# Performance work log

Measured on AMD Instinct MI355X. Metric: run time of the kernel, lower is better.

The kernel has to match this reference:

```python
import jax, jax.numpy as jnp
import numpy as np

BN_EPS = 1e-5
NUM_GRAPHS = 256


def _bn(h, g, b):
    # training-mode batch norm over the node dimension
    m = jnp.mean(h, axis=0)
    v = jnp.var(h, axis=0)
    return g * (h - m) * jax.lax.rsqrt(v + BN_EPS) + b


def setup_inputs() -> dict:
    key = jax.random.key(0)
    ks = jax.random.split(key, 24)
    N, E, F, H, H3 = 50000, 800000, 64, 128, 512
    C, R, L1 = 256, H + H + H3, 1024  # num_classes, readout dim 768, lin1 width

    def w(k, shape):
        return (jax.random.normal(k, shape, jnp.float32) / np.float32(np.sqrt(shape[0])))

    return {
        "x": jax.random.normal(ks[0], (N, F), jnp.float32),
        "edge_index": jax.random.randint(ks[1], (2, E), 0, N, jnp.int32),
        "batch": jnp.sort(jax.random.randint(ks[2], (N,), 0, NUM_GRAPHS, jnp.int32)),
        # conv1 MLP: Linear(F,H) ReLU Linear(H,H); BN1
        "w1a": w(ks[3], (F, H)), "b1a": jnp.zeros((H,), jnp.float32),
        "w1b": w(ks[4], (H, H)), "b1b": jnp.zeros((H,), jnp.float32),
        "g1": jnp.ones((H,), jnp.float32), "bt1": jnp.zeros((H,), jnp.float32),
        # conv2 MLP: Linear(H,H) ReLU Linear(H,H); BN2
        "w2a": w(ks[5], (H, H)), "b2a": jnp.zeros((H,), jnp.float32),
        "w2b": w(ks[6], (H, H)), "b2b": jnp.zeros((H,), jnp.float32),
        "g2": jnp.ones((H,), jnp.float32), "bt2": jnp.zeros((H,), jnp.float32),
        # conv3 MLP: Linear(H,512) ReLU; BN3
        "w3": w(ks[7], (H, H3)), "b3": jnp.zeros((H3,), jnp.float32),
        "g3": jnp.ones((H3,), jnp.float32), "bt3": jnp.zeros((H3,), jnp.float32),
        # readout MLP
        "wl1": w(ks[8], (R, L1)), "bl1": jnp.zeros((L1,), jnp.float32),
        "wl2": w(ks[9], (L1, C)), "bl2": jnp.zeros((C,), jnp.float32),
    }


def reference(x, edge_index, batch,
              w1a, b1a, w1b, b1b, g1, bt1,
              w2a, b2a, w2b, b2b, g2, bt2,
              w3, b3, g3, bt3,
              wl1, bl1, wl2, bl2):
    src, dst = edge_index[0], edge_index[1]
    N = x.shape[0]

    def agg(h):  # GIN aggregation, eps=0: x_i + sum_{j->i} x_j
        return h + jax.ops.segment_sum(h[src], dst, num_segments=N)

    h1 = jax.nn.relu(_bn(jax.nn.relu(agg(x) @ w1a + b1a) @ w1b + b1b, g1, bt1))
    h2 = jax.nn.relu(_bn(jax.nn.relu(agg(h1) @ w2a + b2a) @ w2b + b2b, g2, bt2))
    h3 = jax.nn.relu(_bn(jax.nn.relu(agg(h2) @ w3 + b3), g3, bt3))

    def pool(h):  # global_add_pool
        return jax.ops.segment_sum(h, batch, num_segments=NUM_GRAPHS)

    h = jnp.concatenate([pool(h1), pool(h2), pool(h3)], axis=1)  # [G, 768]
    return jax.nn.relu(h @ wl1 + bl1) @ wl2 + bl2  # [G, num_classes]
```

## Files before the change

### kernel.cpp

```cpp
#include <hip/hip_runtime.h>

#define DEV_INLINE __device__ __forceinline__

DEV_INLINE void fma4(float4& a, float s, const float4& w) {
  a.x = fmaf(s, w.x, a.x);
  a.y = fmaf(s, w.y, a.y);
  a.z = fmaf(s, w.z, a.z);
  a.w = fmaf(s, w.w, a.w);
}

DEV_INLINE float4 xform4(const float4& v, const float4& sc, const float4& sh) {
  float4 r;
  r.x = fmaxf(fmaf(v.x, sc.x, sh.x), 0.f);
  r.y = fmaxf(fmaf(v.y, sc.y, sh.y), 0.f);
  r.z = fmaxf(fmaf(v.z, sc.z, sh.z), 0.f);
  r.w = fmaxf(fmaf(v.w, sc.w, sh.w), 0.f);
  return r;
}

DEV_INLINE void atomAddF(float* p, float v) { unsafeAtomicAdd(p, v); }

__global__ void hist_kernel(const int* __restrict__ dst, int* __restrict__ deg, int E) {
  int i = blockIdx.x * blockDim.x + threadIdx.x;
  int st = gridDim.x * blockDim.x;
  for (; i < E; i += st) atomicAdd(&deg[dst[i]], 1);
}

__global__ __launch_bounds__(1024) void scan_kernel(const int* __restrict__ deg,
                                                    int* __restrict__ rowStart,
                                                    int* __restrict__ cursor, int N) {
  __shared__ int part[1024];
  const int t = threadIdx.x;
  const int chunk = (N + 1023) / 1024;
  const int base = t * chunk;
  int s = 0;
  for (int i = 0; i < chunk; ++i) {
    int idx = base + i;
    if (idx < N) s += deg[idx];
  }
  part[t] = s;
  __syncthreads();
  for (int off = 1; off < 1024; off <<= 1) {
    int u = (t >= off) ? part[t - off] : 0;
    __syncthreads();
    part[t] += u;
    __syncthreads();
  }
  int running = part[t] - s;
  for (int i = 0; i < chunk; ++i) {
    int idx = base + i;
    if (idx < N) {
      rowStart[idx] = running;
      cursor[idx] = running;
      running += deg[idx];
    }
  }
  if (t == 1023) rowStart[N] = part[1023];
}

__global__ void fill_kernel(const int* __restrict__ src, const int* __restrict__ dst,
                            int* __restrict__ cursor, int* __restrict__ adj, int E) {
  int i = blockIdx.x * blockDim.x + threadIdx.x;
  int st = gridDim.x * blockDim.x;
  for (; i < E; i += st) {
    int slot = atomicAdd(&cursor[dst[i]], 1);
    adj[slot] = src[i];
  }
}

template <int CH4, bool XF>
__global__ __launch_bounds__(256) void gather_kernel(const float* __restrict__ h,
                                                     const int* __restrict__ rowStart,
                                                     const int* __restrict__ adj,
                                                     const float* __restrict__ ss,
                                                     float* __restrict__ agg, int N) {
  constexpr int H = CH4 * 4;
  constexpr int NPB = 256 / CH4;
  const int t = threadIdx.x;
  const int c4 = t % CH4;
  const int nl = t / CH4;
  const int node = blockIdx.x * NPB + nl;
  if (node >= N) return;
  const int c = c4 * 4;
  float4 sc, sh;
  if (XF) {
    sc = *reinterpret_cast<const float4*>(ss + c);
    sh = *reinterpret_cast<const float4*>(ss + H + c);
  }
  float4 acc = *reinterpret_cast<const float4*>(h + (long long)node * H + c);
  if (XF) acc = xform4(acc, sc, sh);
  const int e1 = rowStart[node + 1];
  for (int i = rowStart[node]; i < e1; ++i) {
    int s = adj[i];
    float4 u = *reinterpret_cast<const float4*>(h + (long long)s * H + c);
    if (XF) u = xform4(u, sc, sh);
    acc.x += u.x; acc.y += u.y; acc.z += u.z; acc.w += u.w;
  }
  *reinterpret_cast<float4*>(agg + (long long)node * H + c) = acc;
}

template <int K, int NC, bool RELU, bool STATS>
__global__ __launch_bounds__(256) void gemm_kernel(const float* __restrict__ A,
                                                   const float* __restrict__ W,
                                                   const float* __restrict__ bias,
                                                   float* __restrict__ out,
                                                   float* __restrict__ stats, int N) {
  __shared__ float As[64 * 68];
  __shared__ float Ws[64 * 128];
  const int t = threadIdx.x;
  const int tx = t & 31, ty = t >> 5;
  const int row0 = blockIdx.x * 64;
  const int col0 = blockIdx.y * 128;

  float4 acc[8];
#pragma unroll
  for (int i = 0; i < 8; ++i) acc[i] = make_float4(0.f, 0.f, 0.f, 0.f);

  for (int kc = 0; kc < K; kc += 64) {
    __syncthreads();
#pragma unroll
    for (int p = 0; p < 4; ++p) {
      int s = p * 256 + t;
      int r = s >> 4, kq = (s & 15) << 2;
      float4 v = make_float4(0.f, 0.f, 0.f, 0.f);
      if (row0 + r < N)
        v = *reinterpret_cast<const float4*>(A + (long long)(row0 + r) * K + kc + kq);
      *reinterpret_cast<float4*>(As + r * 68 + kq) = v;
    }
#pragma unroll
    for (int p = 0; p < 8; ++p) {
      int s = p * 256 + t;
      int k = s >> 5, c = (s & 31) << 2;
      *reinterpret_cast<float4*>(Ws + k * 128 + c) =
          *reinterpret_cast<const float4*>(W + (long long)(kc + k) * NC + col0 + c);
    }
    __syncthreads();
#pragma unroll
    for (int k4 = 0; k4 < 16; ++k4) {
      float4 w0 = *reinterpret_cast<const float4*>(Ws + (k4 * 4 + 0) * 128 + tx * 4);
      float4 w1 = *reinterpret_cast<const float4*>(Ws + (k4 * 4 + 1) * 128 + tx * 4);
      float4 w2 = *reinterpret_cast<const float4*>(Ws + (k4 * 4 + 2) * 128 + tx * 4);
      float4 w3 = *reinterpret_cast<const float4*>(Ws + (k4 * 4 + 3) * 128 + tx * 4);
#pragma unroll
      for (int i = 0; i < 8; ++i) {
        float4 a = *reinterpret_cast<const float4*>(As + (ty * 8 + i) * 68 + k4 * 4);
        fma4(acc[i], a.x, w0);
        fma4(acc[i], a.y, w1);
        fma4(acc[i], a.z, w2);
        fma4(acc[i], a.w, w3);
      }
    }
  }

  const float4 b4 = *reinterpret_cast<const float4*>(bias + col0 + tx * 4);
  float ps[4] = {0.f, 0.f, 0.f, 0.f}, pq[4] = {0.f, 0.f, 0.f, 0.f};
#pragma unroll
  for (int i = 0; i < 8; ++i) {
    int row = row0 + ty * 8 + i;
    float4 v = acc[i];
    v.x += b4.x; v.y += b4.y; v.z += b4.z; v.w += b4.w;
    if (RELU) {
      v.x = fmaxf(v.x, 0.f); v.y = fmaxf(v.y, 0.f);
      v.z = fmaxf(v.z, 0.f); v.w = fmaxf(v.w, 0.f);
    }
    if (row < N) {
      *reinterpret_cast<float4*>(out + (long long)row * NC + col0 + tx * 4) = v;
      if (STATS) {
        ps[0] += v.x; ps[1] += v.y; ps[2] += v.z; ps[3] += v.w;
        pq[0] += v.x * v.x; pq[1] += v.y * v.y; pq[2] += v.z * v.z; pq[3] += v.w * v.w;
      }
    }
  }
  if (STATS) {
    __syncthreads();
    float* r1 = As;
    float* r2 = As + 1024;
#pragma unroll
    for (int j = 0; j < 4; ++j) {
      r1[ty * 128 + tx * 4 + j] = ps[j];
      r2[ty * 128 + tx * 4 + j] = pq[j];
    }
    __syncthreads();
    if (t < 128) {
      float s = 0.f, s2 = 0.f;
#pragma unroll
      for (int q = 0; q < 8; ++q) { s += r1[q * 128 + t]; s2 += r2[q * 128 + t]; }
      atomAddF(&stats[col0 + t], s);
      atomAddF(&stats[NC + col0 + t], s2);
    }
  }
}

__global__ void bn_finalize_kernel(const float* __restrict__ stats, const float* __restrict__ g,
                                   const float* __restrict__ b, float* __restrict__ ss, int C,
                                   float invN) {
  int c = blockIdx.x * blockDim.x + threadIdx.x;
  if (c < C) {
    float mean = stats[c] * invN;
    float var = stats[C + c] * invN - mean * mean;
    float rstd = rsqrtf(var + 1e-5f);
    float scale = g[c] * rstd;
    ss[c] = scale;
    ss[C + c] = b[c] - mean * scale;
  }
}

template <int C, bool XF>
__global__ void pool_kernel(const float* __restrict__ h, const int* __restrict__ batch,
                            const float* __restrict__ ss, float* __restrict__ pooled, int N,
                            int colOff) {
  constexpr int CH4 = C / 4;
  constexpr int RPG = 256 / CH4;
  const int g = blockIdx.x;
  const int t = threadIdx.x;
  int lo = 0, hi = N;
  while (lo < hi) { int m = (lo + hi) >> 1; if (batch[m] < g) lo = m + 1; else hi = m; }
  const int rs = lo;
  hi = N;
  while (lo < hi) { int m = (lo + hi) >> 1; if (batch[m] <= g) lo = m + 1; else hi = m; }
  const int re = lo;

  const int c = (t % CH4) * 4;
  const int rp = t / CH4;
  float4 sc, sh;
  if (XF) {
    sc = *reinterpret_cast<const float4*>(ss + c);
    sh = *reinterpret_cast<const float4*>(ss + C + c);
  }
  float4 acc = make_float4(0.f, 0.f, 0.f, 0.f);
  for (int r = rs + rp; r < re; r += RPG) {
    float4 v = *reinterpret_cast<const float4*>(h + (long long)r * C + c);
    if (XF) v = xform4(v, sc, sh);
    acc.x += v.x; acc.y += v.y; acc.z += v.z; acc.w += v.w;
  }
  __shared__ float4 red[256];
  red[t] = acc;
  __syncthreads();
  if (t < CH4) {
    float4 s = red[t];
#pragma unroll
    for (int q = 1; q < RPG; ++q) {
      float4 v = red[q * CH4 + t];
      s.x += v.x; s.y += v.y; s.z += v.z; s.w += v.w;
    }
    *reinterpret_cast<float4*>(pooled + g * 768 + colOff + t * 4) = s;
  }
}

template <bool RELU>
__global__ __launch_bounds__(256) void small_gemm_kernel(const float* __restrict__ A,
                                                         const float* __restrict__ W,
                                                         const float* __restrict__ bias,
                                                         float* __restrict__ out, int K, int NC) {
  const int t = threadIdx.x;
  const int tx = t & 15, rl = t >> 4;
  const int row = blockIdx.x * 16 + rl;
  const int col = blockIdx.y * 64 + tx * 4;
  const float* a = A + (long long)row * K;
  const float* w = W + col;
  float4 acc = make_float4(0.f, 0.f, 0.f, 0.f);
  for (int k = 0; k < K; k += 4) {
    float4 a4 = *reinterpret_cast<const float4*>(a + k);
    float4 w0 = *reinterpret_cast<const float4*>(w + (long long)(k + 0) * NC);
    float4 w1 = *reinterpret_cast<const float4*>(w + (long long)(k + 1) * NC);
    float4 w2 = *reinterpret_cast<const float4*>(w + (long long)(k + 2) * NC);
    float4 w3 = *reinterpret_cast<const float4*>(w + (long long)(k + 3) * NC);
    fma4(acc, a4.x, w0);
    fma4(acc, a4.y, w1);
    fma4(acc, a4.z, w2);
    fma4(acc, a4.w, w3);
  }
  float4 b4 = *reinterpret_cast<const float4*>(bias + col);
  acc.x += b4.x; acc.y += b4.y; acc.z += b4.z; acc.w += b4.w;
  if (RELU) {
    acc.x = fmaxf(acc.x, 0.f); acc.y = fmaxf(acc.y, 0.f);
    acc.z = fmaxf(acc.z, 0.f); acc.w = fmaxf(acc.w, 0.f);
  }
  *reinterpret_cast<float4*>(out + (long long)row * NC + col) = acc;
}

static inline int imin_(int a, int b) { return a < b ? a : b; }
static inline int cdiv_(long long a, long long b) { return (int)((a + b - 1) / b); }

extern "C" void kernel_launch(void* const* d_in, const int* in_sizes, int n_in,
                              void* d_out, int out_size, void* d_ws, size_t ws_size,
                              hipStream_t stream) {
  const int N = in_sizes[0] / 64;
  const int E = in_sizes[1] / 2;
  const float* x = (const float*)d_in[0];
  const int* ei = (const int*)d_in[1];
  const int* batch = (const int*)d_in[2];
  const float *w1a = (const float*)d_in[3], *b1a = (const float*)d_in[4];
  const float *w1b = (const float*)d_in[5], *b1b = (const float*)d_in[6];
  const float *g1 = (const float*)d_in[7], *bt1 = (const float*)d_in[8];
  const float *w2a = (const float*)d_in[9], *b2a = (const float*)d_in[10];
  const float *w2b = (const float*)d_in[11], *b2b = (const float*)d_in[12];
  const float *g2 = (const float*)d_in[13], *bt2 = (const float*)d_in[14];
  const float *w3 = (const float*)d_in[15], *b3 = (const float*)d_in[16];
  const float *g3 = (const float*)d_in[17], *bt3 = (const float*)d_in[18];
  const float *wl1 = (const float*)d_in[19], *bl1 = (const float*)d_in[20];
  const float *wl2 = (const float*)d_in[21], *bl2 = (const float*)d_in[22];
  const int* src = ei;
  const int* dst = ei + E;

  float* ws = (float*)d_ws;
  float* buf0 = ws;
  float* buf1 = buf0 + (size_t)N * 128;
  float* buf2 = buf1 + (size_t)N * 128;
  float* buf3 = buf2 + (size_t)N * 128;
  float* pooled = buf3 + (size_t)N * 512;
  float* l1 = pooled + 256 * 768;
  float* sums = l1 + 256 * 1024;
  float* ssb = sums + 1536;

  int* rowStart = (int*)buf3;
  int* cursor = rowStart + (N + 1);
  int* adj = cursor + N;
  int* deg = adj + E;

  hipMemsetAsync(sums, 0, 1536 * sizeof(float), stream);
  hipMemsetAsync(deg, 0, (size_t)N * sizeof(int), stream);

  const int NB = (N + 63) / 64;
  const float invN = 1.0f / (float)N;
  float* ss1 = ssb;
  float* ss2 = ssb + 256;
  float* ss3 = ssb + 512;

  hist_kernel<<<imin_(cdiv_(E, 256), 8192), 256, 0, stream>>>(dst, deg, E);
  scan_kernel<<<1, 1024, 0, stream>>>(deg, rowStart, cursor, N);
  fill_kernel<<<imin_(cdiv_(E, 256), 8192), 256, 0, stream>>>(src, dst, cursor, adj, E);

  gather_kernel<16, false><<<cdiv_(N, 16), 256, 0, stream>>>(x, rowStart, adj, nullptr, buf0, N);
  gemm_kernel<64, 128, true, false><<<dim3(NB, 1), 256, 0, stream>>>(buf0, w1a, b1a, buf1, nullptr, N);
  gemm_kernel<128, 128, false, true><<<dim3(NB, 1), 256, 0, stream>>>(buf1, w1b, b1b, buf2, sums, N);
  bn_finalize_kernel<<<1, 128, 0, stream>>>(sums, g1, bt1, ss1, 128, invN);
  pool_kernel<128, true><<<256, 256, 0, stream>>>(buf2, batch, ss1, pooled, N, 0);

  gather_kernel<32, true><<<cdiv_(N, 8), 256, 0, stream>>>(buf2, rowStart, adj, ss1, buf1, N);
  gemm_kernel<128, 128, true, false><<<dim3(NB, 1), 256, 0, stream>>>(buf1, w2a, b2a, buf0, nullptr, N);
  gemm_kernel<128, 128, false, true><<<dim3(NB, 1), 256, 0, stream>>>(buf0, w2b, b2b, buf2, sums + 256, N);
  bn_finalize_kernel<<<1, 128, 0, stream>>>(sums + 256, g2, bt2, ss2, 128, invN);
  pool_kernel<128, true><<<256, 256, 0, stream>>>(buf2, batch, ss2, pooled, N, 128);

  gather_kernel<32, true><<<cdiv_(N, 8), 256, 0, stream>>>(buf2, rowStart, adj, ss2, buf1, N);
  gemm_kernel<128, 512, true, true><<<dim3(NB, 4), 256, 0, stream>>>(buf1, w3, b3, buf3, sums + 512, N);
  bn_finalize_kernel<<<1, 512, 0, stream>>>(sums + 512, g3, bt3, ss3, 512, invN);
  pool_kernel<512, true><<<256, 256, 0, stream>>>(buf3, batch, ss3, pooled, N, 256);

  small_gemm_kernel<true><<<dim3(16, 16), 256, 0, stream>>>(pooled, wl1, bl1, l1, 768, 1024);
  small_gemm_kernel<false><<<dim3(16, 4), 256, 0, stream>>>(l1, wl2, bl2, (float*)d_out, 1024, 256);
}
```

Measured before the change: 1.129 ms.

## Unroll gather loop, add GEMM occupancy hint, split pooling across slices with atomics

The neighbor gather loop now handles two edges per iteration, so two independent row loads are in flight at once. The GEMM gets a launch-bounds minimum-blocks hint and keeps its K loop rolled, aiming for more resident blocks per CU. Pooling is split across 4 or 8 row slices per graph, with partial sums combined by float atomics into a zero-initialized pooled buffer, which raises parallelism from 256 blocks. This adds a memset plus atomic traffic and makes the summation order nondeterministic.

```diff
diff --git a/kernel.cpp b/kernel.cpp
--- a/kernel.cpp
+++ b/kernel.cpp
@@ -90,21 +90,30 @@
   float4 acc = *reinterpret_cast<const float4*>(h + (long long)node * H + c);
   if (XF) acc = xform4(acc, sc, sh);
   const int e1 = rowStart[node + 1];
-  for (int i = rowStart[node]; i < e1; ++i) {
-    int s = adj[i];
-    float4 u = *reinterpret_cast<const float4*>(h + (long long)s * H + c);
-    if (XF) u = xform4(u, sc, sh);
-    acc.x += u.x; acc.y += u.y; acc.z += u.z; acc.w += u.w;
+  int i = rowStart[node];
+  for (; i + 1 < e1; i += 2) {
+    int s0 = adj[i], s1 = adj[i + 1];
+    float4 u0 = *reinterpret_cast<const float4*>(h + (long long)s0 * H + c);
+    float4 u1 = *reinterpret_cast<const float4*>(h + (long long)s1 * H + c);
+    if (XF) { u0 = xform4(u0, sc, sh); u1 = xform4(u1, sc, sh); }
+    acc.x += u0.x + u1.x; acc.y += u0.y + u1.y;
+    acc.z += u0.z + u1.z; acc.w += u0.w + u1.w;
+  }
+  if (i < e1) {
+    int s0 = adj[i];
+    float4 u0 = *reinterpret_cast<const float4*>(h + (long long)s0 * H + c);
+    if (XF) u0 = xform4(u0, sc, sh);
+    acc.x += u0.x; acc.y += u0.y; acc.z += u0.z; acc.w += u0.w;
   }
   *reinterpret_cast<float4*>(agg + (long long)node * H + c) = acc;
 }
 
 template <int K, int NC, bool RELU, bool STATS>
-__global__ __launch_bounds__(256) void gemm_kernel(const float* __restrict__ A,
-                                                   const float* __restrict__ W,
-                                                   const float* __restrict__ bias,
-                                                   float* __restrict__ out,
-                                                   float* __restrict__ stats, int N) {
+__global__ __launch_bounds__(256, 3) void gemm_kernel(const float* __restrict__ A,
+                                                      const float* __restrict__ W,
+                                                      const float* __restrict__ bias,
+                                                      float* __restrict__ out,
+                                                      float* __restrict__ stats, int N) {
   __shared__ float As[64 * 68];
   __shared__ float Ws[64 * 128];
   const int t = threadIdx.x;
@@ -116,6 +125,7 @@
 #pragma unroll
   for (int i = 0; i < 8; ++i) acc[i] = make_float4(0.f, 0.f, 0.f, 0.f);
 
+#pragma unroll 1
   for (int kc = 0; kc < K; kc += 64) {
     __syncthreads();
 #pragma unroll
@@ -205,13 +215,14 @@
   }
 }
 
-template <int C, bool XF>
+template <int C, bool XF, int S>
 __global__ void pool_kernel(const float* __restrict__ h, const int* __restrict__ batch,
                             const float* __restrict__ ss, float* __restrict__ pooled, int N,
                             int colOff) {
   constexpr int CH4 = C / 4;
   constexpr int RPG = 256 / CH4;
   const int g = blockIdx.x;
+  const int slice = blockIdx.y;
   const int t = threadIdx.x;
   int lo = 0, hi = N;
   while (lo < hi) { int m = (lo + hi) >> 1; if (batch[m] < g) lo = m + 1; else hi = m; }
@@ -228,7 +239,7 @@
     sh = *reinterpret_cast<const float4*>(ss + C + c);
   }
   float4 acc = make_float4(0.f, 0.f, 0.f, 0.f);
-  for (int r = rs + rp; r < re; r += RPG) {
+  for (int r = rs + rp + slice * RPG; r < re; r += RPG * S) {
     float4 v = *reinterpret_cast<const float4*>(h + (long long)r * C + c);
     if (XF) v = xform4(v, sc, sh);
     acc.x += v.x; acc.y += v.y; acc.z += v.z; acc.w += v.w;
@@ -243,7 +254,11 @@
       float4 v = red[q * CH4 + t];
       s.x += v.x; s.y += v.y; s.z += v.z; s.w += v.w;
     }
-    *reinterpret_cast<float4*>(pooled + g * 768 + colOff + t * 4) = s;
+    float* p = pooled + g * 768 + colOff + t * 4;
+    atomAddF(p + 0, s.x);
+    atomAddF(p + 1, s.y);
+    atomAddF(p + 2, s.z);
+    atomAddF(p + 3, s.w);
   }
 }
 
@@ -320,6 +335,7 @@
 
   hipMemsetAsync(sums, 0, 1536 * sizeof(float), stream);
   hipMemsetAsync(deg, 0, (size_t)N * sizeof(int), stream);
+  hipMemsetAsync(pooled, 0, 256 * 768 * sizeof(float), stream);
 
   const int NB = (N + 63) / 64;
   const float invN = 1.0f / (float)N;
@@ -335,18 +351,18 @@
   gemm_kernel<64, 128, true, false><<<dim3(NB, 1), 256, 0, stream>>>(buf0, w1a, b1a, buf1, nullptr, N);
   gemm_kernel<128, 128, false, true><<<dim3(NB, 1), 256, 0, stream>>>(buf1, w1b, b1b, buf2, sums, N);
   bn_finalize_kernel<<<1, 128, 0, stream>>>(sums, g1, bt1, ss1, 128, invN);
-  pool_kernel<128, true><<<256, 256, 0, stream>>>(buf2, batch, ss1, pooled, N, 0);
+  pool_kernel<128, true, 4><<<dim3(256, 4), 256, 0, stream>>>(buf2, batch, ss1, pooled, N, 0);
 
   gather_kernel<32, true><<<cdiv_(N, 8), 256, 0, stream>>>(buf2, rowStart, adj, ss1, buf1, N);
   gemm_kernel<128, 128, true, false><<<dim3(NB, 1), 256, 0, stream>>>(buf1, w2a, b2a, buf0, nullptr, N);
   gemm_kernel<128, 128, false, true><<<dim3(NB, 1), 256, 0, stream>>>(buf0, w2b, b2b, buf2, sums + 256, N);
   bn_finalize_kernel<<<1, 128, 0, stream>>>(sums + 256, g2, bt2, ss2, 128, invN);
-  pool_kernel<128, true><<<256, 256, 0, stream>>>(buf2, batch, ss2, pooled, N, 128);
+  pool_kernel<128, true, 4><<<dim3(256, 4), 256, 0, stream>>>(buf2, batch, ss2, pooled, N, 128);
 
   gather_kernel<32, true><<<cdiv_(N, 8), 256, 0, stream>>>(buf2, rowStart, adj, ss2, buf1, N);
   gemm_kernel<128, 512, true, true><<<dim3(NB, 4), 256, 0, stream>>>(buf1, w3, b3, buf3, sums + 512, N);
   bn_finalize_kernel<<<1, 512, 0, stream>>>(sums + 512, g3, bt3, ss3, 512, invN);
-  pool_kernel<512, true><<<256, 256, 0, stream>>>(buf3, batch, ss3, pooled, N, 256);
+  pool_kernel<512, true, 8><<<dim3(256, 8), 256, 0, stream>>>(buf3, batch, ss3, pooled, N, 256);
 
   small_gemm_kernel<true><<<dim3(16, 16), 256, 0, stream>>>(pooled, wl1, bl1, l1, 768, 1024);
   small_gemm_kernel<false><<<dim3(16, 4), 256, 0, stream>>>(l1, wl2, bl2, (float*)d_out, 1024, 256);
```

Result: slower. 1.361 ms (+20.6%).
